# Kernel optimization log

Measured on AMD Instinct MI355X. Metric: run time of the kernel, lower is better.

Reference implementation:

```python
import jax, jax.numpy as jnp
import numpy as np

B, NPQ, NPV, NSL, K, ED, H = 64, 1024, 256, 1, 128, 16, 8
DK = K // H  # per-head dim (k_dim = v_dim = emb_dim // num_heads)
ETYPES = [("PQ","PQ"),("PQ","PV"),("PQ","Slack"),("PV","PQ"),("PV","PV"),("PV","Slack"),("Slack","PQ"),("Slack","PV")]
ECOUNTS = [262144, 131072, 4096, 131072, 65536, 2048, 4096, 2048]
NN = {"PQ": B*NPQ, "PV": B*NPV, "Slack": B*NSL}
LN_EPS = 1e-5


def setup_inputs() -> dict:
    ks = iter(jax.random.split(jax.random.key(0), 64))
    inp = {}
    for name, n in [("x_PQ", NN["PQ"]), ("x_PV", NN["PV"]), ("x_Slack", NN["Slack"])]:
        inp[name] = jax.random.normal(next(ks), (n, K), jnp.float32)
    for t, ((s, d), E) in enumerate(zip(ETYPES, ECOUNTS)):
        src = jax.random.randint(next(ks), (E,), 0, NN[s])
        dst = jax.random.randint(next(ks), (E,), 0, NN[d])
        inp[f"ei_{t}"] = jnp.stack([src, dst]).astype(jnp.int32)
        inp[f"ea_{t}"] = jax.random.normal(next(ks), (E, ED), jnp.float32)
    sc = 1.0 / np.sqrt(K)
    shapes = {"Wk": (2,8,K,K), "bk": (2,8,K), "Wq": (2,8,K,K), "bq": (2,8,K),
              "Wv": (2,8,K,K), "bv": (2,8,K), "Ws": (2,8,K,K), "bconv": (2,8,K),
              "We": (2,8,ED,K), "be": (2,8,K), "Wgt": (K,K), "bgt": (K,),
              "Wq1": (K,K), "Wk2": (K,K), "Wv2": (K,K), "Wo": (K,K), "bo": (K,)}
    for name, sh in shapes.items():
        inp[name] = jax.random.normal(next(ks), sh, jnp.float32) * sc
    inp["ln_g"] = jnp.ones((K,), jnp.float32)
    inp["ln_b"] = jnp.zeros((K,), jnp.float32)
    return inp


def _cross_attention(x1, x2, Wq1, Wk2, Wv2, Wo, bo):
    # x1: [B, N1, K] queries; x2: [B, N2, K] keys/values
    Bq, N1, _ = x1.shape
    N2 = x2.shape[1]
    q = (x1 @ Wq1).reshape(Bq, N1, H, DK)
    k = (x2 @ Wk2).reshape(Bq, N2, H, DK)
    v = (x2 @ Wv2).reshape(Bq, N2, H, DK)
    attn = jnp.einsum("bnhd,bmhd->bhnm", q, k) / np.sqrt(DK).astype(np.float32)
    attn = jax.nn.softmax(attn, axis=-1)
    out = jnp.einsum("bhnm,bmhd->bnhd", attn, v).reshape(Bq, N1, H * DK)
    return out @ Wo + bo


def _forward(x_PQ, x_PV, x_Slack, ei, ea,
             Wk, bk, Wq, bq, Wv, bv, Ws, bconv, We, be,
             Wgt, bgt, Wq1, Wk2, Wv2, Wo, bo, ln_g, ln_b):
    x = {"PQ": x_PQ, "PV": x_PV, "Slack": x_Slack}
    # global feature from input node features
    gf = jnp.concatenate([x_PQ.reshape(B, NPQ, K),
                          x_PV.reshape(B, NPV, K),
                          x_Slack.reshape(B, NSL, K)], axis=1)
    gf = gf @ Wgt + bgt
    gnode = jnp.concatenate([gf.mean(axis=1, keepdims=True),
                             gf.max(axis=1, keepdims=True)], axis=1)  # [B, 2, K]
    # 2 HeteroConv layers of ResGatedGraphConv, aggr='sum' over edge types
    for l in range(2):
        new = {t: jnp.zeros((NN[t], K), x_PQ.dtype) for t in ("PQ", "PV", "Slack")}
        for t, (s, d) in enumerate(ETYPES):
            xs, xd = x[s], x[d]
            k_ = xd @ Wk[l, t] + bk[l, t]   # lin_key on dst
            q_ = xs @ Wq[l, t] + bq[l, t]   # lin_query on src
            v_ = xs @ Wv[l, t] + bv[l, t]   # lin_value on src
            e_ = ea[t] @ We[l, t] + be[l, t]  # lin_edge
            si, di = ei[t][0], ei[t][1]
            gate = jax.nn.sigmoid(k_[di] + q_[si] + e_)  # [E, K]
            agg = jax.ops.segment_sum(gate * v_[si], di, num_segments=NN[d])
            new[d] = new[d] + agg + xd @ Ws[l, t] + bconv[l, t]
        x = {t: jax.nn.relu(v) for t, v in new.items()}
    # cross-attention vs. global mean/max nodes, residual, layernorm (PQ, PV only)
    res = {}
    for key2, N1 in (("PQ", NPQ), ("PV", NPV)):
        x1 = x[key2].reshape(B, N1, K)
        ca = _cross_attention(x1, gnode, Wq1, Wk2, Wv2, Wo, bo).reshape(B * N1, K)
        h = x[key2] + ca
        mu = h.mean(axis=-1, keepdims=True)
        var = ((h - mu) ** 2).mean(axis=-1, keepdims=True)
        res[key2] = (h - mu) * jax.lax.rsqrt(var + LN_EPS) * ln_g + ln_b
    return res["PQ"], res["PV"], x["Slack"]


def reference(x_PQ, x_PV, x_Slack,
              ei_0, ei_1, ei_2, ei_3, ei_4, ei_5, ei_6, ei_7,
              ea_0, ea_1, ea_2, ea_3, ea_4, ea_5, ea_6, ea_7,
              Wk, bk, Wq, bq, Wv, bv, Ws, bconv, We, be,
              Wgt, bgt, Wq1, Wk2, Wv2, Wo, bo, ln_g, ln_b):
    ei = [ei_0, ei_1, ei_2, ei_3, ei_4, ei_5, ei_6, ei_7]
    ea = [ea_0, ea_1, ea_2, ea_3, ea_4, ea_5, ea_6, ea_7]
    return _forward(x_PQ, x_PV, x_Slack, ei, ea,
                    Wk, bk, Wq, bq, Wv, bv, Ws, bconv, We, be,
                    Wgt, bgt, Wq1, Wk2, Wv2, Wo, bo, ln_g, ln_b)
```

## Files before the change

kernel.cpp:

```cpp
#include <hip/hip_runtime.h>
#include <hip/hip_bf16.h>
#include <math.h>

#define N_PQ 65536
#define N_PV 16384
#define N_SL 64

typedef __attribute__((ext_vector_type(8))) short s16x8;
typedef __attribute__((ext_vector_type(4))) float f32x4;

__device__ __forceinline__ ushort f2bf(float f) {
    union { float f; unsigned u; } x; x.f = f;
    unsigned r = x.u + 0x7fff + ((x.u >> 16) & 1);
    return (ushort)(r >> 16);
}
__device__ __forceinline__ float bf2f(ushort u) {
    union { unsigned u; float f; } x; x.u = ((unsigned)u) << 16;
    return x.f;
}

template<int OUT_BF16>
__global__ __launch_bounds__(256) void gemm_mfma(
    const ushort* __restrict__ A, const ushort* __restrict__ Bt,
    const float* __restrict__ bias, void* __restrict__ Cv, int M, int N)
{
    __shared__ ushort As[128 * 128];
    const int tid = threadIdx.x;
    const int m0 = blockIdx.x * 128;
    const int n0 = blockIdx.y * 128;

    #pragma unroll
    for (int p = 0; p < 8; ++p) {
        int c = p * 256 + tid;
        int row = c >> 4, c16 = c & 15;
        int gr = m0 + row;
        int4 v = make_int4(0, 0, 0, 0);
        if (gr < M) v = *(const int4*)(A + (size_t)gr * 128 + c16 * 8);
        *(int4*)(As + row * 128 + (c16 ^ (row & 7)) * 8) = v;
    }
    __syncthreads();

    const int lane = tid & 63, wave = tid >> 6;
    const int wr = wave >> 1, wc = wave & 1;
    const int lrow = lane & 15, lk = lane >> 4;

    f32x4 acc[4][4];
    #pragma unroll
    for (int mi = 0; mi < 4; ++mi)
        #pragma unroll
        for (int ni = 0; ni < 4; ++ni) acc[mi][ni] = (f32x4){0.f, 0.f, 0.f, 0.f};

    #pragma unroll
    for (int kk = 0; kk < 4; ++kk) {
        s16x8 a[4], b[4];
        #pragma unroll
        for (int mi = 0; mi < 4; ++mi) {
            int row = wr * 64 + mi * 16 + lrow;
            int c16 = (lk + kk * 4) ^ (row & 7);
            a[mi] = *(const s16x8*)(As + row * 128 + c16 * 8);
        }
        #pragma unroll
        for (int ni = 0; ni < 4; ++ni) {
            int n = n0 + wc * 64 + ni * 16 + lrow;
            b[ni] = *(const s16x8*)(Bt + (size_t)n * 128 + kk * 32 + lk * 8);
        }
        #pragma unroll
        for (int mi = 0; mi < 4; ++mi)
            #pragma unroll
            for (int ni = 0; ni < 4; ++ni)
                acc[mi][ni] = __builtin_amdgcn_mfma_f32_16x16x32_bf16(
                    a[mi], b[ni], acc[mi][ni], 0, 0, 0);
    }

    if (OUT_BF16) {
        __syncthreads();
        ushort* Cl = As;
        #pragma unroll
        for (int mi = 0; mi < 4; ++mi)
            #pragma unroll
            for (int ni = 0; ni < 4; ++ni)
                #pragma unroll
                for (int r = 0; r < 4; ++r) {
                    int row = wr * 64 + mi * 16 + (lane >> 4) * 4 + r;
                    int col = wc * 64 + ni * 16 + (lane & 15);
                    float v = acc[mi][ni][r] + (bias ? bias[n0 + col] : 0.f);
                    Cl[row * 128 + (((col >> 3) ^ (row & 7)) << 3) + (col & 7)] = f2bf(v);
                }
        __syncthreads();
        ushort* C = (ushort*)Cv;
        #pragma unroll
        for (int p = 0; p < 8; ++p) {
            int c = p * 256 + tid;
            int row = c >> 4, c16 = c & 15;
            int gr = m0 + row;
            if (gr < M)
                *(int4*)(C + (size_t)gr * N + n0 + c16 * 8) =
                    *(const int4*)(As + row * 128 + (c16 ^ (row & 7)) * 8);
        }
    } else {
        float* C = (float*)Cv;
        #pragma unroll
        for (int mi = 0; mi < 4; ++mi)
            #pragma unroll
            for (int ni = 0; ni < 4; ++ni)
                #pragma unroll
                for (int r = 0; r < 4; ++r) {
                    int row = m0 + wr * 64 + mi * 16 + (lane >> 4) * 4 + r;
                    int col = n0 + wc * 64 + ni * 16 + (lane & 15);
                    if (row < M)
                        C[(size_t)row * N + col] =
                            acc[mi][ni][r] + (bias ? bias[col] : 0.f);
                }
    }
}

__global__ void prep_mats(
    const float* __restrict__ Wk, const float* __restrict__ Wq,
    const float* __restrict__ Wv, const float* __restrict__ Ws,
    const float* __restrict__ Wgt, const float* __restrict__ Wq1,
    const float* __restrict__ Wk2, const float* __restrict__ Wv2,
    const float* __restrict__ Wo,
    ushort* __restrict__ panels, ushort* __restrict__ wssum,
    ushort* __restrict__ finalw)
{
    const int m = blockIdx.x >> 6;
    const int e = (blockIdx.x & 63) * 256 + threadIdx.x;
    const int nl = e >> 7, k = e & 127;
    const int dstlist[3][3] = {{0,3,6},{1,4,7},{2,5,-1}};
    const int srclist[3][3] = {{0,1,2},{3,4,5},{6,7,-1}};
    const int nkg[3] = {3,3,2};
    const int gofs[3] = {0,1280,2560};

    if (m < 52) {
        int l = m / 26, r = m % 26;
        int g, slot;
        if (r < 10)      { g = 0; slot = r; }
        else if (r < 20) { g = 1; slot = r - 10; }
        else             { g = 2; slot = r - 20; }
        int nk = nkg[g];
        float val; int col;
        if (slot < nk) {
            int t = dstlist[g][slot];
            val = Wk[(size_t)(l * 8 + t) * 16384 + k * 128 + nl];
            col = slot * 128 + nl;
        } else if (slot < 2 * nk) {
            int s = slot - nk; int t = srclist[g][s];
            val = Wq[(size_t)(l * 8 + t) * 16384 + k * 128 + nl];
            col = nk * 128 + s * 256 + ((nl >> 1) << 2) + (nl & 1);
        } else if (slot < 3 * nk) {
            int s = slot - 2 * nk; int t = srclist[g][s];
            val = Wv[(size_t)(l * 8 + t) * 16384 + k * 128 + nl];
            col = nk * 128 + s * 256 + ((nl >> 1) << 2) + 2 + (nl & 1);
        } else {
            float s = 0.f;
            #pragma unroll
            for (int i = 0; i < 3; ++i) {
                int t = dstlist[g][i];
                if (t >= 0) s += Ws[(size_t)(l * 8 + t) * 16384 + k * 128 + nl];
            }
            val = s; col = 1152 + nl;
        }
        panels[((size_t)l * 3328 + gofs[g] + col) * 128 + k] = f2bf(val);
    } else if (m < 54) {
        int l = m - 52;
        float s = Ws[(size_t)(l * 8 + 2) * 16384 + k * 128 + nl]
                + Ws[(size_t)(l * 8 + 5) * 16384 + k * 128 + nl];
        wssum[(size_t)l * 16384 + nl * 128 + k] = f2bf(s);
    } else {
        const float* fsrc[5] = {Wgt, Wq1, Wk2, Wv2, Wo};
        int idx = m - 54;
        finalw[(size_t)idx * 16384 + nl * 128 + k] = f2bf(fsrc[idx][k * 128 + nl]);
    }
}

__global__ void prep_bias(
    const float* __restrict__ bk, const float* __restrict__ bq,
    const float* __restrict__ bv, const float* __restrict__ bconv,
    float* __restrict__ bias_cat, float* __restrict__ bcsum)
{
    const int l = blockIdx.x / 3, g = blockIdx.x % 3;
    const int dstlist[3][3] = {{0,3,6},{1,4,7},{2,5,-1}};
    const int srclist[3][3] = {{0,1,2},{3,4,5},{6,7,-1}};
    const int nkg[3] = {3,3,2};
    const int gofs[3] = {0,1280,2560};
    const int nslots = (g < 2) ? 10 : 6;
    int nk = nkg[g];
    for (int idx = threadIdx.x; idx < nslots * 128; idx += 256) {
        int slot = idx >> 7, nl = idx & 127;
        float val; int col;
        if (slot < nk) {
            int t = dstlist[g][slot];
            val = bk[(l * 8 + t) * 128 + nl];
            col = slot * 128 + nl;
        } else if (slot < 2 * nk) {
            int s = slot - nk; int t = srclist[g][s];
            val = bq[(l * 8 + t) * 128 + nl];
            col = nk * 128 + s * 256 + ((nl >> 1) << 2) + (nl & 1);
        } else if (slot < 3 * nk) {
            int s = slot - 2 * nk; int t = srclist[g][s];
            val = bv[(l * 8 + t) * 128 + nl];
            col = nk * 128 + s * 256 + ((nl >> 1) << 2) + 2 + (nl & 1);
        } else {
            float s = 0.f;
            #pragma unroll
            for (int i = 0; i < 3; ++i) {
                int t = dstlist[g][i];
                if (t >= 0) s += bconv[(l * 8 + t) * 128 + nl];
            }
            val = s; col = 1152 + nl;
        }
        bias_cat[l * 3328 + gofs[g] + col] = val;
    }
    if (g == 2 && threadIdx.x < 128) {
        bcsum[l * 128 + threadIdx.x] =
            bconv[(l * 8 + 2) * 128 + threadIdx.x] + bconv[(l * 8 + 5) * 128 + threadIdx.x];
    }
}

struct HArgs {
    const int* ei[6];
    int E[6];
    int base[6];
    int cum[7];
};

__global__ void hist_kernel(HArgs A, int* __restrict__ bins)
{
    int g = blockIdx.x * 256 + threadIdx.x;
    if (g >= A.cum[6]) return;
    int t = 0;
    #pragma unroll
    for (int i = 0; i < 5; ++i) t += (g >= A.cum[i + 1]);
    int e = g - A.cum[t];
    int dst = A.ei[t][A.E[t] + e];
    atomicAdd(&bins[A.base[t] + dst], 1);
}

__global__ __launch_bounds__(256) void scan_a(
    const int* __restrict__ bins, int* __restrict__ offs, int* __restrict__ bsum)
{
    __shared__ int s[256];
    const int b = blockIdx.x, t = threadIdx.x;
    int v = bins[b * 256 + t];
    s[t] = v; __syncthreads();
    #pragma unroll
    for (int off = 1; off < 256; off <<= 1) {
        int x = (t >= off) ? s[t - off] : 0;
        __syncthreads();
        s[t] += x;
        __syncthreads();
    }
    offs[b * 256 + t] = s[t] - v;
    if (t == 255) bsum[b] = s[255];
}

__global__ __launch_bounds__(1024) void scan_b(
    const int* __restrict__ bsum, int* __restrict__ carry)
{
    __shared__ int s[1024];
    const int t = threadIdx.x;
    int v = bsum[t];
    s[t] = v; __syncthreads();
    for (int off = 1; off < 1024; off <<= 1) {
        int x = (t >= off) ? s[t - off] : 0;
        __syncthreads();
        s[t] += x;
        __syncthreads();
    }
    carry[t] = s[t] - v;
}

__global__ void scan_c(int* __restrict__ offs, const int* __restrict__ carry,
                       int* __restrict__ cursor)
{
    const int b = blockIdx.x, t = threadIdx.x;
    int v = offs[b * 256 + t] + carry[b];
    offs[b * 256 + t] = v;
    cursor[b * 256 + t] = v;
}

__global__ void scatter_kernel(HArgs A, int* __restrict__ cursor,
                               int* __restrict__ lsrc, int* __restrict__ leid)
{
    int g = blockIdx.x * 256 + threadIdx.x;
    if (g >= A.cum[6]) return;
    int t = 0;
    #pragma unroll
    for (int i = 0; i < 5; ++i) t += (g >= A.cum[i + 1]);
    int e = g - A.cum[t];
    int src = A.ei[t][e];
    int dst = A.ei[t][A.E[t] + e];
    int pos = atomicAdd(&cursor[A.base[t] + dst], 1);
    lsrc[pos] = src;
    leid[pos] = e;
}

struct GTA {
    int base, kcol, qvcol, lds;
    const ushort* Ys;
    const float* ea;
    const float* We;
    const float* be;
};
struct GArgs {
    GTA t[3];
    const int* offs;
    const int* lsrc;
    const int* leid;
    ushort* xbg;
    const ushort* Yg;
    int ldg, wscol;
};

__global__ __launch_bounds__(256) void gather_kernel(GArgs A)
{
    const int wave = threadIdx.x >> 6, lane = threadIdx.x & 63;
    const int d = blockIdx.x * 4 + wave;
    const int j0 = lane * 2;

    ushort2 w2 = *(const ushort2*)(A.Yg + (size_t)d * A.ldg + A.wscol + j0);
    float a0 = bf2f(w2.x), a1 = bf2f(w2.y);

    #pragma unroll
    for (int i = 0; i < 3; ++i) {
        const GTA T = A.t[i];
        int start = __builtin_amdgcn_readfirstlane(A.offs[T.base + d]);
        int end   = __builtin_amdgcn_readfirstlane(A.offs[T.base + d + 1]);
        if (start == end) continue;

        ushort2 kk = *(const ushort2*)(A.Yg + (size_t)d * A.ldg + T.kcol + j0);
        float k0 = bf2f(kk.x), k1 = bf2f(kk.y);
        float we0[16], we1[16];
        #pragma unroll
        for (int r = 0; r < 16; ++r) {
            float2 wv = *(const float2*)(T.We + r * 128 + j0);
            we0[r] = wv.x; we1[r] = wv.y;
        }
        float2 be2 = *(const float2*)(T.be + j0);

        int si  = __builtin_amdgcn_readfirstlane(A.lsrc[start]);
        int eid = __builtin_amdgcn_readfirstlane(A.leid[start]);
        uint2 qv = *(const uint2*)(T.Ys + (size_t)si * T.lds + T.qvcol + lane * 4);
        float4 eA = *(const float4*)(T.ea + (size_t)eid * 16);
        float4 eB = *(const float4*)(T.ea + (size_t)eid * 16 + 4);
        float4 eC = *(const float4*)(T.ea + (size_t)eid * 16 + 8);
        float4 eD = *(const float4*)(T.ea + (size_t)eid * 16 + 12);

        for (int e = start; e < end; ++e) {
            int nx = (e + 1 < end) ? (e + 1) : e;
            int si_n  = __builtin_amdgcn_readfirstlane(A.lsrc[nx]);
            int eid_n = __builtin_amdgcn_readfirstlane(A.leid[nx]);
            uint2 qv_n = *(const uint2*)(T.Ys + (size_t)si_n * T.lds + T.qvcol + lane * 4);
            float4 nA = *(const float4*)(T.ea + (size_t)eid_n * 16);
            float4 nB = *(const float4*)(T.ea + (size_t)eid_n * 16 + 4);
            float4 nC = *(const float4*)(T.ea + (size_t)eid_n * 16 + 8);
            float4 nD = *(const float4*)(T.ea + (size_t)eid_n * 16 + 12);

            float e0 = be2.x, e1 = be2.y;
            e0 += eA.x*we0[0] + eA.y*we0[1] + eA.z*we0[2] + eA.w*we0[3]
                + eB.x*we0[4] + eB.y*we0[5] + eB.z*we0[6] + eB.w*we0[7]
                + eC.x*we0[8] + eC.y*we0[9] + eC.z*we0[10] + eC.w*we0[11]
                + eD.x*we0[12] + eD.y*we0[13] + eD.z*we0[14] + eD.w*we0[15];
            e1 += eA.x*we1[0] + eA.y*we1[1] + eA.z*we1[2] + eA.w*we1[3]
                + eB.x*we1[4] + eB.y*we1[5] + eB.z*we1[6] + eB.w*we1[7]
                + eC.x*we1[8] + eC.y*we1[9] + eC.z*we1[10] + eC.w*we1[11]
                + eD.x*we1[12] + eD.y*we1[13] + eD.z*we1[14] + eD.w*we1[15];
            float q0 = bf2f((ushort)(qv.x & 0xffff)), q1 = bf2f((ushort)(qv.x >> 16));
            float v0 = bf2f((ushort)(qv.y & 0xffff)), v1 = bf2f((ushort)(qv.y >> 16));
            float g0 = 1.f / (1.f + __expf(-(k0 + q0 + e0)));
            float g1 = 1.f / (1.f + __expf(-(k1 + q1 + e1)));
            a0 += g0 * v0;
            a1 += g1 * v1;
            qv = qv_n; eA = nA; eB = nB; eC = nC; eD = nD;
        }
    }
    ushort2 o; o.x = f2bf(fmaxf(a0, 0.f)); o.y = f2bf(fmaxf(a1, 0.f));
    *(ushort2*)(A.xbg + (size_t)d * 128 + j0) = o;
}

__global__ __launch_bounds__(256) void edge_slack(
    const int* __restrict__ ei, const float* __restrict__ ea,
    const float* __restrict__ We, const float* __restrict__ be,
    const ushort* __restrict__ Yk, int ldk,
    const ushort* __restrict__ Yqv, int ldq,
    float* __restrict__ nd, int E)
{
    const int e = blockIdx.x * 2 + (threadIdx.x >> 7);
    if (e >= E) return;
    const int j = threadIdx.x & 127;
    const int si = ei[e];
    const int di = ei[E + e];

    float ej = be[j];
    #pragma unroll
    for (int r = 0; r < 16; ++r)
        ej += ea[(size_t)e * 16 + r] * We[r * 128 + j];

    float kv = bf2f(Yk[(size_t)di * ldk + j]);
    float qv = bf2f(Yqv[(size_t)si * ldq + ((j >> 1) << 2) + (j & 1)]);
    float vv = bf2f(Yqv[(size_t)si * ldq + ((j >> 1) << 2) + 2 + (j & 1)]);
    float g  = 1.f / (1.f + __expf(-(kv + qv + ej)));
    atomicAdd(&nd[(size_t)di * 128 + j], g * vv);
}

__global__ void f2b_kernel(const float* __restrict__ a, ushort* __restrict__ o, int n)
{
    int i = (blockIdx.x * 256 + threadIdx.x) * 4;
    if (i < n) {
        float4 v = *(const float4*)(a + i);
        ushort4 u; u.x = f2bf(v.x); u.y = f2bf(v.y); u.z = f2bf(v.z); u.w = f2bf(v.w);
        *(ushort4*)(o + i) = u;
    }
}
__global__ void relu_b_kernel(const float* __restrict__ a, ushort* __restrict__ o, int n)
{
    int i = (blockIdx.x * 256 + threadIdx.x) * 4;
    if (i < n) {
        float4 v = *(const float4*)(a + i);
        ushort4 u;
        u.x = f2bf(fmaxf(v.x, 0.f)); u.y = f2bf(fmaxf(v.y, 0.f));
        u.z = f2bf(fmaxf(v.z, 0.f)); u.w = f2bf(fmaxf(v.w, 0.f));
        *(ushort4*)(o + i) = u;
    }
}
__global__ void b2f_kernel(const ushort* __restrict__ a, float* __restrict__ o, int n)
{
    int i = blockIdx.x * 256 + threadIdx.x;
    if (i < n) o[i] = bf2f(a[i]);
}

__global__ void pool1(const ushort* __restrict__ gf, float* __restrict__ pbuf)
{
    const int b = blockIdx.x >> 4, c = blockIdx.x & 15;
    const int j = threadIdx.x;
    float s = 0.f, m = -INFINITY;
    const ushort* pq = gf + (size_t)(b * 1024 + c * 64) * 128;
    for (int i = 0; i < 64; ++i) { float v = bf2f(pq[i * 128 + j]); s += v; m = fmaxf(m, v); }
    const ushort* pv = gf + (size_t)(N_PQ + b * 256 + c * 16) * 128;
    for (int i = 0; i < 16; ++i) { float v = bf2f(pv[i * 128 + j]); s += v; m = fmaxf(m, v); }
    if (c == 0) { float v = bf2f(gf[(size_t)(N_PQ + N_PV + b) * 128 + j]); s += v; m = fmaxf(m, v); }
    pbuf[(size_t)blockIdx.x * 256 + j] = s;
    pbuf[(size_t)blockIdx.x * 256 + 128 + j] = m;
}
__global__ void pool2(const float* __restrict__ pbuf, float* __restrict__ gnode)
{
    const int b = blockIdx.x, j = threadIdx.x;
    float s = 0.f, m = -INFINITY;
    for (int c = 0; c < 16; ++c) {
        s += pbuf[(size_t)(b * 16 + c) * 256 + j];
        m = fmaxf(m, pbuf[(size_t)(b * 16 + c) * 256 + 128 + j]);
    }
    gnode[(size_t)(b * 2) * 128 + j]     = s * (1.f / 1281.f);
    gnode[(size_t)(b * 2 + 1) * 128 + j] = m;
}

__global__ __launch_bounds__(256) void attn_kernel(
    const ushort* __restrict__ q, const float* __restrict__ k2,
    const float* __restrict__ v2, ushort* __restrict__ ao, int shift, int Ntot)
{
    const int n = blockIdx.x * 2 + (threadIdx.x >> 7);
    if (n >= Ntot) return;
    const int j = threadIdx.x & 127;
    const int b = n >> shift;
    const int h16 = j & ~15;

    const ushort* qn = q + (size_t)n * 128 + h16;
    const float* k0 = k2 + (size_t)(b * 2) * 128 + h16;
    const float* k1 = k2 + (size_t)(b * 2 + 1) * 128 + h16;
    float s0 = 0.f, s1 = 0.f;
    #pragma unroll
    for (int d = 0; d < 16; ++d) {
        float qq = bf2f(qn[d]); s0 += qq * k0[d]; s1 += qq * k1[d];
    }
    s0 *= 0.25f; s1 *= 0.25f;
    float m  = fmaxf(s0, s1);
    float a0 = __expf(s0 - m), a1 = __expf(s1 - m);
    float inv = 1.f / (a0 + a1);
    ao[(size_t)n * 128 + j] = f2bf(
        (a0 * v2[(size_t)(b * 2) * 128 + j] + a1 * v2[(size_t)(b * 2 + 1) * 128 + j]) * inv);
}

__global__ __launch_bounds__(256) void ln_kernel(
    const ushort* __restrict__ x, const float* __restrict__ ca,
    const float* __restrict__ g, const float* __restrict__ bb,
    float* __restrict__ out, int N)
{
    const int n = blockIdx.x * 4 + (threadIdx.x >> 6);
    if (n >= N) return;
    const int l = threadIdx.x & 63;
    const size_t base = (size_t)n * 128;
    float h0 = bf2f(x[base + l * 2])     + ca[base + l * 2];
    float h1 = bf2f(x[base + l * 2 + 1]) + ca[base + l * 2 + 1];
    float s  = h0 + h1;
    float ss = h0 * h0 + h1 * h1;
    #pragma unroll
    for (int o = 32; o; o >>= 1) { s += __shfl_xor(s, o); ss += __shfl_xor(ss, o); }
    float mu  = s * (1.f / 128.f);
    float var = ss * (1.f / 128.f) - mu * mu;
    float rs  = rsqrtf(var + 1e-5f);
    out[base + l * 2]     = (h0 - mu) * rs * g[l * 2]     + bb[l * 2];
    out[base + l * 2 + 1] = (h1 - mu) * rs * g[l * 2 + 1] + bb[l * 2 + 1];
}

extern "C" void kernel_launch(void* const* d_in, const int* in_sizes, int n_in,
                              void* d_out, int out_size, void* d_ws, size_t ws_size,
                              hipStream_t stream)
{
    const float* xin[3] = {(const float*)d_in[0], (const float*)d_in[1], (const float*)d_in[2]};
    const int NNs[3] = {N_PQ, N_PV, N_SL};
    const int ncol[3] = {1280, 1280, 768};
    const int gofs[3] = {0, 1280, 2560};

    const int*   ei[8];
    const float* ea[8];
    int          Ecnt[8];
    for (int t = 0; t < 8; ++t) {
        ei[t]   = (const int*)d_in[3 + 2 * t];
        ea[t]   = (const float*)d_in[4 + 2 * t];
        Ecnt[t] = in_sizes[3 + 2 * t] / 2;
    }
    const float* Wk    = (const float*)d_in[19];
    const float* bk    = (const float*)d_in[20];
    const float* Wq    = (const float*)d_in[21];
    const float* bq    = (const float*)d_in[22];
    const float* Wv    = (const float*)d_in[23];
    const float* bv    = (const float*)d_in[24];
    const float* Ws    = (const float*)d_in[25];
    const float* bconv = (const float*)d_in[26];
    const float* We    = (const float*)d_in[27];
    const float* be    = (const float*)d_in[28];
    const float* Wgt   = (const float*)d_in[29];
    const float* bgt   = (const float*)d_in[30];
    const float* Wq1   = (const float*)d_in[31];
    const float* Wk2   = (const float*)d_in[32];
    const float* Wv2   = (const float*)d_in[33];
    const float* Wo    = (const float*)d_in[34];
    const float* bo    = (const float*)d_in[35];
    const float* ln_g  = (const float*)d_in[36];
    const float* ln_b  = (const float*)d_in[37];

    char* w = (char*)d_ws;
    ushort* Y[3];
    Y[0] = (ushort*)w; w += (size_t)N_PQ * 1280 * 2;
    Y[1] = (ushort*)w; w += (size_t)N_PV * 1280 * 2;
    Y[2] = (ushort*)w; w += (size_t)N_SL * 768 * 2;
    ushort* xb[3];
    xb[0] = (ushort*)w; w += (size_t)N_PQ * 128 * 2;
    xb[1] = (ushort*)w; w += (size_t)N_PV * 128 * 2;
    xb[2] = (ushort*)w; w += (size_t)N_SL * 128 * 2;
    ushort* panels = (ushort*)w; w += (size_t)2 * 3328 * 128 * 2;
    ushort* wssum  = (ushort*)w; w += (size_t)2 * 16384 * 2;
    ushort* finalw = (ushort*)w; w += (size_t)5 * 16384 * 2;
    float* bias_cat = (float*)w; w += 6656 * 4;
    float* bcsum    = (float*)w; w += 256 * 4;
    float* gnode    = (float*)w; w += 16384 * 4;
    ushort* gnodeb  = (ushort*)w; w += 16384 * 2;
    float* k2       = (float*)w; w += 16384 * 4;
    float* v2       = (float*)w; w += 16384 * 4;
    float* pbuf     = (float*)w; w += 1024 * 256 * 4;
    const int NBINS = 262144;
    int* bins   = (int*)w; w += (size_t)NBINS * 4;
    int* offs   = (int*)w; w += (size_t)NBINS * 4;
    int* cursor = (int*)w; w += (size_t)NBINS * 4;
    int* bsum   = (int*)w; w += 1024 * 4;
    int* carry  = (int*)w; w += 1024 * 4;
    int* lsrc   = (int*)w; w += (size_t)600064 * 4;
    int* leid   = (int*)w; w += (size_t)600064 * 4;
    ushort* gf   = Y[0];
    ushort* qb   = Y[0];
    ushort* ao   = (ushort*)((char*)Y[0] + (size_t)N_PQ * 128 * 2);
    float*  cbuf = (float*)((char*)Y[0] + (size_t)N_PQ * 128 * 4);
    float* outp = (float*)d_out;
    float* nw2 = outp + (size_t)(N_PQ + N_PV) * 128;

    const ushort* Wgt_t = finalw;
    const ushort* Wq1_t = finalw + 16384;
    const ushort* Wk2_t = finalw + 32768;
    const ushort* Wv2_t = finalw + 49152;
    const ushort* Wo_t  = finalw + 65536;

    auto gemm_b = [&](const ushort* A, const ushort* Bt, const float* bias,
                      ushort* C, int M, int N) {
        gemm_mfma<1><<<dim3((M + 127) / 128, N / 128), 256, 0, stream>>>(A, Bt, bias, C, M, N);
    };
    auto gemm_f = [&](const ushort* A, const ushort* Bt, const float* bias,
                      float* C, int M, int N) {
        gemm_mfma<0><<<dim3((M + 127) / 128, N / 128), 256, 0, stream>>>(A, Bt, bias, C, M, N);
    };

    prep_mats<<<59 * 64, 256, 0, stream>>>(Wk, Wq, Wv, Ws, Wgt, Wq1, Wk2, Wv2, Wo,
                                           panels, wssum, finalw);
    prep_bias<<<6, 256, 0, stream>>>(bk, bq, bv, bconv, bias_cat, bcsum);
    for (int g = 0; g < 3; ++g) {
        int n = NNs[g] * 128;
        f2b_kernel<<<dim3((n / 4 + 255) / 256), 256, 0, stream>>>(xin[g], xb[g], n);
    }

    const int csr_t[6]    = {0, 3, 6, 1, 4, 7};
    const int csr_base[6] = {0, 65536, 131072, 196608, 212992, 229376};
    HArgs ha;
    {
        int c = 0;
        for (int i = 0; i < 6; ++i) {
            int t = csr_t[i];
            ha.ei[i] = ei[t]; ha.E[i] = Ecnt[t]; ha.base[i] = csr_base[i];
            ha.cum[i] = c; c += Ecnt[t];
        }
        ha.cum[6] = c;
    }
    hipMemsetAsync(bins, 0, (size_t)NBINS * 4, stream);
    hist_kernel<<<dim3((ha.cum[6] + 255) / 256), 256, 0, stream>>>(ha, bins);
    scan_a<<<1024, 256, 0, stream>>>(bins, offs, bsum);
    scan_b<<<1, 1024, 0, stream>>>(bsum, carry);
    scan_c<<<1024, 256, 0, stream>>>(offs, carry, cursor);
    scatter_kernel<<<dim3((ha.cum[6] + 255) / 256), 256, 0, stream>>>(ha, cursor, lsrc, leid);

    gemm_b(xb[0], Wgt_t, bgt, gf, N_PQ, 128);
    gemm_b(xb[1], Wgt_t, bgt, gf + (size_t)N_PQ * 128, N_PV, 128);
    gemm_b(xb[2], Wgt_t, bgt, gf + (size_t)(N_PQ + N_PV) * 128, N_SL, 128);
    pool1<<<1024, 128, 0, stream>>>(gf, pbuf);
    pool2<<<64, 128, 0, stream>>>(pbuf, gnode);
    f2b_kernel<<<dim3(16384 / 4 / 256), 256, 0, stream>>>(gnode, gnodeb, 16384);
    gemm_f(gnodeb, Wk2_t, nullptr, k2, 128, 128);
    gemm_f(gnodeb, Wv2_t, nullptr, v2, 128, 128);

    for (int l = 0; l < 2; ++l) {
        for (int g = 0; g < 3; ++g)
            gemm_b(xb[g], panels + ((size_t)l * 3328 + gofs[g]) * 128,
                   bias_cat + l * 3328 + gofs[g], Y[g], NNs[g], ncol[g]);
        gemm_f(xb[2], wssum + (size_t)l * 16384, bcsum + l * 128, nw2, N_SL, 128);

        for (int g = 0; g < 2; ++g) {
            GArgs ga;
            for (int i = 0; i < 3; ++i) {
                int t = csr_t[g * 3 + i], off = l * 8 + t;
                int sgrp = (i == 2) ? 2 : i;
                ga.t[i].base  = csr_base[g * 3 + i];
                ga.t[i].kcol  = i * 128;
                ga.t[i].lds   = ncol[sgrp];
                ga.t[i].qvcol = ((sgrp == 2) ? 256 : 384) + g * 256;
                ga.t[i].Ys    = Y[sgrp];
                ga.t[i].ea    = ea[t];
                ga.t[i].We    = We + (size_t)off * 2048;
                ga.t[i].be    = be + (size_t)off * 128;
            }
            ga.offs = offs; ga.lsrc = lsrc; ga.leid = leid;
            ga.xbg = xb[g]; ga.Yg = Y[g]; ga.ldg = ncol[g]; ga.wscol = 1152;
            gather_kernel<<<dim3(NNs[g] / 4), 256, 0, stream>>>(ga);
        }

        {
            int off2 = l * 8 + 2;
            edge_slack<<<dim3((Ecnt[2] + 1) / 2), 256, 0, stream>>>(
                ei[2], ea[2], We + (size_t)off2 * 2048, be + (size_t)off2 * 128,
                Y[2] + 0, 768, Y[0] + 896, 1280, nw2, Ecnt[2]);
            int off5 = l * 8 + 5;
            edge_slack<<<dim3((Ecnt[5] + 1) / 2), 256, 0, stream>>>(
                ei[5], ea[5], We + (size_t)off5 * 2048, be + (size_t)off5 * 128,
                Y[2] + 128, 768, Y[1] + 896, 1280, nw2, Ecnt[5]);
        }
        relu_b_kernel<<<dim3(8), 256, 0, stream>>>(nw2, xb[2], N_SL * 128);
    }

    gemm_b(xb[0], Wq1_t, nullptr, qb, N_PQ, 128);
    attn_kernel<<<dim3(N_PQ / 2), 256, 0, stream>>>(qb, k2, v2, ao, 10, N_PQ);
    gemm_f(ao, Wo_t, bo, cbuf, N_PQ, 128);
    ln_kernel<<<dim3(N_PQ / 4), 256, 0, stream>>>(xb[0], cbuf, ln_g, ln_b, outp, N_PQ);
    gemm_b(xb[1], Wq1_t, nullptr, qb, N_PV, 128);
    attn_kernel<<<dim3(N_PV / 2), 256, 0, stream>>>(qb, k2, v2, ao, 8, N_PV);
    gemm_f(ao, Wo_t, bo, cbuf, N_PV, 128);
    ln_kernel<<<dim3(N_PV / 4), 256, 0, stream>>>(xb[1], cbuf, ln_g, ln_b,
                                                  outp + (size_t)N_PQ * 128, N_PV);
    b2f_kernel<<<dim3((N_SL * 128 + 255) / 256), 256, 0, stream>>>(
        xb[2], outp + (size_t)(N_PQ + N_PV) * 128, N_SL * 128);
}
```

Measured before the change: 985.1 us.

## Widen GEMM N-tile, pack CSR src/eid pairs, stage edge weights in LDS

When N is a multiple of 256, the bf16-output GEMM now computes two 128-column tiles per block, so the A tile loaded into LDS is reused across more output columns. The CSR source and edge-id arrays are merged into one int2 array, so each edge needs a single index load. The gather kernel now stages all three edge-type We matrices in LDS instead of holding them in registers, and reads edge attributes per iteration rather than prefetching them. The trade-offs are doubled accumulator register pressure in the GEMM, 24 KB of LDS per gather block, and ea loads that are no longer prefetched one edge ahead.

```diff
diff --git a/kernel.cpp b/kernel.cpp
--- a/kernel.cpp
+++ b/kernel.cpp
@@ -19,7 +19,7 @@
     return x.f;
 }
 
-template<int OUT_BF16>
+template<int OUT_BF16, int NT>
 __global__ __launch_bounds__(256) void gemm_mfma(
     const ushort* __restrict__ A, const ushort* __restrict__ Bt,
     const float* __restrict__ bias, void* __restrict__ Cv, int M, int N)
@@ -27,7 +27,7 @@
     __shared__ ushort As[128 * 128];
     const int tid = threadIdx.x;
     const int m0 = blockIdx.x * 128;
-    const int n0 = blockIdx.y * 128;
+    const int n0 = blockIdx.y * (128 * NT);
 
     #pragma unroll
     for (int p = 0; p < 8; ++p) {
@@ -44,15 +44,15 @@
     const int wr = wave >> 1, wc = wave & 1;
     const int lrow = lane & 15, lk = lane >> 4;
 
-    f32x4 acc[4][4];
+    f32x4 acc[4][4 * NT];
     #pragma unroll
     for (int mi = 0; mi < 4; ++mi)
         #pragma unroll
-        for (int ni = 0; ni < 4; ++ni) acc[mi][ni] = (f32x4){0.f, 0.f, 0.f, 0.f};
+        for (int ni = 0; ni < 4 * NT; ++ni) acc[mi][ni] = (f32x4){0.f, 0.f, 0.f, 0.f};
 
     #pragma unroll
     for (int kk = 0; kk < 4; ++kk) {
-        s16x8 a[4], b[4];
+        s16x8 a[4], b[4 * NT];
         #pragma unroll
         for (int mi = 0; mi < 4; ++mi) {
             int row = wr * 64 + mi * 16 + lrow;
@@ -60,53 +60,57 @@
             a[mi] = *(const s16x8*)(As + row * 128 + c16 * 8);
         }
         #pragma unroll
-        for (int ni = 0; ni < 4; ++ni) {
-            int n = n0 + wc * 64 + ni * 16 + lrow;
+        for (int ni = 0; ni < 4 * NT; ++ni) {
+            int n = n0 + (ni >> 2) * 128 + wc * 64 + (ni & 3) * 16 + lrow;
             b[ni] = *(const s16x8*)(Bt + (size_t)n * 128 + kk * 32 + lk * 8);
         }
         #pragma unroll
         for (int mi = 0; mi < 4; ++mi)
             #pragma unroll
-            for (int ni = 0; ni < 4; ++ni)
+            for (int ni = 0; ni < 4 * NT; ++ni)
                 acc[mi][ni] = __builtin_amdgcn_mfma_f32_16x16x32_bf16(
                     a[mi], b[ni], acc[mi][ni], 0, 0, 0);
     }
 
     if (OUT_BF16) {
-        __syncthreads();
-        ushort* Cl = As;
         #pragma unroll
-        for (int mi = 0; mi < 4; ++mi)
+        for (int s = 0; s < NT; ++s) {
+            __syncthreads();
+            ushort* Cl = As;
             #pragma unroll
-            for (int ni = 0; ni < 4; ++ni)
+            for (int mi = 0; mi < 4; ++mi)
                 #pragma unroll
-                for (int r = 0; r < 4; ++r) {
-                    int row = wr * 64 + mi * 16 + (lane >> 4) * 4 + r;
-                    int col = wc * 64 + ni * 16 + (lane & 15);
-                    float v = acc[mi][ni][r] + (bias ? bias[n0 + col] : 0.f);
-                    Cl[row * 128 + (((col >> 3) ^ (row & 7)) << 3) + (col & 7)] = f2bf(v);
-                }
-        __syncthreads();
-        ushort* C = (ushort*)Cv;
-        #pragma unroll
-        for (int p = 0; p < 8; ++p) {
-            int c = p * 256 + tid;
-            int row = c >> 4, c16 = c & 15;
-            int gr = m0 + row;
-            if (gr < M)
-                *(int4*)(C + (size_t)gr * N + n0 + c16 * 8) =
-                    *(const int4*)(As + row * 128 + (c16 ^ (row & 7)) * 8);
+                for (int q = 0; q < 4; ++q)
+                    #pragma unroll
+                    for (int r = 0; r < 4; ++r) {
+                        int row = wr * 64 + mi * 16 + (lane >> 4) * 4 + r;
+                        int col = wc * 64 + q * 16 + (lane & 15);
+                        float v = acc[mi][s * 4 + q][r]
+                                + (bias ? bias[n0 + s * 128 + col] : 0.f);
+                        Cl[row * 128 + (((col >> 3) ^ (row & 7)) << 3) + (col & 7)] = f2bf(v);
+                    }
+            __syncthreads();
+            ushort* C = (ushort*)Cv;
+            #pragma unroll
+            for (int p = 0; p < 8; ++p) {
+                int c = p * 256 + tid;
+                int row = c >> 4, c16 = c & 15;
+                int gr = m0 + row;
+                if (gr < M)
+                    *(int4*)(C + (size_t)gr * N + n0 + s * 128 + c16 * 8) =
+                        *(const int4*)(As + row * 128 + (c16 ^ (row & 7)) * 8);
+            }
         }
     } else {
         float* C = (float*)Cv;
         #pragma unroll
         for (int mi = 0; mi < 4; ++mi)
             #pragma unroll
-            for (int ni = 0; ni < 4; ++ni)
+            for (int ni = 0; ni < 4 * NT; ++ni)
                 #pragma unroll
                 for (int r = 0; r < 4; ++r) {
                     int row = m0 + wr * 64 + mi * 16 + (lane >> 4) * 4 + r;
-                    int col = n0 + wc * 64 + ni * 16 + (lane & 15);
+                    int col = n0 + (ni >> 2) * 128 + wc * 64 + (ni & 3) * 16 + (lane & 15);
                     if (row < M)
                         C[(size_t)row * N + col] =
                             acc[mi][ni][r] + (bias ? bias[col] : 0.f);
@@ -280,7 +284,7 @@
 }
 
 __global__ void scatter_kernel(HArgs A, int* __restrict__ cursor,
-                               int* __restrict__ lsrc, int* __restrict__ leid)
+                               int2* __restrict__ lpair)
 {
     int g = blockIdx.x * 256 + threadIdx.x;
     if (g >= A.cum[6]) return;
@@ -291,8 +295,7 @@
     int src = A.ei[t][e];
     int dst = A.ei[t][A.E[t] + e];
     int pos = atomicAdd(&cursor[A.base[t] + dst], 1);
-    lsrc[pos] = src;
-    leid[pos] = e;
+    lpair[pos] = make_int2(src, e);
 }
 
 struct GTA {
@@ -305,8 +308,7 @@
 struct GArgs {
     GTA t[3];
     const int* offs;
-    const int* lsrc;
-    const int* leid;
+    const int2* lpair;
     ushort* xbg;
     const ushort* Yg;
     int ldg, wscol;
@@ -314,7 +316,13 @@
 
 __global__ __launch_bounds__(256) void gather_kernel(GArgs A)
 {
-    const int wave = threadIdx.x >> 6, lane = threadIdx.x & 63;
+    __shared__ float ldsWe[3 * 16 * 128];
+    const int tid = threadIdx.x;
+    for (int idx = tid; idx < 3 * 2048; idx += 256)
+        ldsWe[idx] = A.t[idx >> 11].We[idx & 2047];
+    __syncthreads();
+
+    const int wave = tid >> 6, lane = tid & 63;
     const int d = blockIdx.x * 4 + wave;
     const int j0 = lane * 2;
 
@@ -330,48 +338,37 @@
 
         ushort2 kk = *(const ushort2*)(A.Yg + (size_t)d * A.ldg + T.kcol + j0);
         float k0 = bf2f(kk.x), k1 = bf2f(kk.y);
-        float we0[16], we1[16];
-        #pragma unroll
-        for (int r = 0; r < 16; ++r) {
-            float2 wv = *(const float2*)(T.We + r * 128 + j0);
-            we0[r] = wv.x; we1[r] = wv.y;
-        }
         float2 be2 = *(const float2*)(T.be + j0);
-
-        int si  = __builtin_amdgcn_readfirstlane(A.lsrc[start]);
-        int eid = __builtin_amdgcn_readfirstlane(A.leid[start]);
+        const float* Wl = ldsWe + i * 2048;
+
+        int2 pr = A.lpair[start];
+        int si  = __builtin_amdgcn_readfirstlane(pr.x);
+        int eid = __builtin_amdgcn_readfirstlane(pr.y);
         uint2 qv = *(const uint2*)(T.Ys + (size_t)si * T.lds + T.qvcol + lane * 4);
-        float4 eA = *(const float4*)(T.ea + (size_t)eid * 16);
-        float4 eB = *(const float4*)(T.ea + (size_t)eid * 16 + 4);
-        float4 eC = *(const float4*)(T.ea + (size_t)eid * 16 + 8);
-        float4 eD = *(const float4*)(T.ea + (size_t)eid * 16 + 12);
 
         for (int e = start; e < end; ++e) {
+            const float* eap = T.ea + (size_t)eid * 16;
+            uint2 qv_c = qv;
             int nx = (e + 1 < end) ? (e + 1) : e;
-            int si_n  = __builtin_amdgcn_readfirstlane(A.lsrc[nx]);
-            int eid_n = __builtin_amdgcn_readfirstlane(A.leid[nx]);
-            uint2 qv_n = *(const uint2*)(T.Ys + (size_t)si_n * T.lds + T.qvcol + lane * 4);
-            float4 nA = *(const float4*)(T.ea + (size_t)eid_n * 16);
-            float4 nB = *(const float4*)(T.ea + (size_t)eid_n * 16 + 4);
-            float4 nC = *(const float4*)(T.ea + (size_t)eid_n * 16 + 8);
-            float4 nD = *(const float4*)(T.ea + (size_t)eid_n * 16 + 12);
+            int2 prn = A.lpair[nx];
+            int si_n = __builtin_amdgcn_readfirstlane(prn.x);
+            eid = __builtin_amdgcn_readfirstlane(prn.y);
+            qv = *(const uint2*)(T.Ys + (size_t)si_n * T.lds + T.qvcol + lane * 4);
 
             float e0 = be2.x, e1 = be2.y;
-            e0 += eA.x*we0[0] + eA.y*we0[1] + eA.z*we0[2] + eA.w*we0[3]
-                + eB.x*we0[4] + eB.y*we0[5] + eB.z*we0[6] + eB.w*we0[7]
-                + eC.x*we0[8] + eC.y*we0[9] + eC.z*we0[10] + eC.w*we0[11]
-                + eD.x*we0[12] + eD.y*we0[13] + eD.z*we0[14] + eD.w*we0[15];
-            e1 += eA.x*we1[0] + eA.y*we1[1] + eA.z*we1[2] + eA.w*we1[3]
-                + eB.x*we1[4] + eB.y*we1[5] + eB.z*we1[6] + eB.w*we1[7]
-                + eC.x*we1[8] + eC.y*we1[9] + eC.z*we1[10] + eC.w*we1[11]
-                + eD.x*we1[12] + eD.y*we1[13] + eD.z*we1[14] + eD.w*we1[15];
-            float q0 = bf2f((ushort)(qv.x & 0xffff)), q1 = bf2f((ushort)(qv.x >> 16));
-            float v0 = bf2f((ushort)(qv.y & 0xffff)), v1 = bf2f((ushort)(qv.y >> 16));
+            #pragma unroll
+            for (int r = 0; r < 16; ++r) {
+                float er = eap[r];
+                float2 wv = *(const float2*)(Wl + r * 128 + j0);
+                e0 = fmaf(er, wv.x, e0);
+                e1 = fmaf(er, wv.y, e1);
+            }
+            float q0 = bf2f((ushort)(qv_c.x & 0xffff)), q1 = bf2f((ushort)(qv_c.x >> 16));
+            float v0 = bf2f((ushort)(qv_c.y & 0xffff)), v1 = bf2f((ushort)(qv_c.y >> 16));
             float g0 = 1.f / (1.f + __expf(-(k0 + q0 + e0)));
             float g1 = 1.f / (1.f + __expf(-(k1 + q1 + e1)));
-            a0 += g0 * v0;
-            a1 += g1 * v1;
-            qv = qv_n; eA = nA; eB = nB; eC = nC; eD = nD;
+            a0 = fmaf(g0, v0, a0);
+            a1 = fmaf(g1, v1, a1);
         }
     }
     ushort2 o; o.x = f2bf(fmaxf(a0, 0.f)); o.y = f2bf(fmaxf(a1, 0.f));
@@ -564,8 +561,7 @@
     int* cursor = (int*)w; w += (size_t)NBINS * 4;
     int* bsum   = (int*)w; w += 1024 * 4;
     int* carry  = (int*)w; w += 1024 * 4;
-    int* lsrc   = (int*)w; w += (size_t)600064 * 4;
-    int* leid   = (int*)w; w += (size_t)600064 * 4;
+    int2* lpair = (int2*)w; w += (size_t)600064 * 8;
     ushort* gf   = Y[0];
     ushort* qb   = Y[0];
     ushort* ao   = (ushort*)((char*)Y[0] + (size_t)N_PQ * 128 * 2);
@@ -581,11 +577,17 @@
 
     auto gemm_b = [&](const ushort* A, const ushort* Bt, const float* bias,
                       ushort* C, int M, int N) {
-        gemm_mfma<1><<<dim3((M + 127) / 128, N / 128), 256, 0, stream>>>(A, Bt, bias, C, M, N);
+        if (N % 256 == 0)
+            gemm_mfma<1, 2><<<dim3((M + 127) / 128, N / 256), 256, 0, stream>>>(
+                A, Bt, bias, C, M, N);
+        else
+            gemm_mfma<1, 1><<<dim3((M + 127) / 128, N / 128), 256, 0, stream>>>(
+                A, Bt, bias, C, M, N);
     };
     auto gemm_f = [&](const ushort* A, const ushort* Bt, const float* bias,
                       float* C, int M, int N) {
-        gemm_mfma<0><<<dim3((M + 127) / 128, N / 128), 256, 0, stream>>>(A, Bt, bias, C, M, N);
+        gemm_mfma<0, 1><<<dim3((M + 127) / 128, N / 128), 256, 0, stream>>>(
+            A, Bt, bias, C, M, N);
     };
 
     prep_mats<<<59 * 64, 256, 0, stream>>>(Wk, Wq, Wv, Ws, Wgt, Wq1, Wk2, Wv2, Wo,
@@ -613,7 +615,7 @@
     scan_a<<<1024, 256, 0, stream>>>(bins, offs, bsum);
     scan_b<<<1, 1024, 0, stream>>>(bsum, carry);
     scan_c<<<1024, 256, 0, stream>>>(offs, carry, cursor);
-    scatter_kernel<<<dim3((ha.cum[6] + 255) / 256), 256, 0, stream>>>(ha, cursor, lsrc, leid);
+    scatter_kernel<<<dim3((ha.cum[6] + 255) / 256), 256, 0, stream>>>(ha, cursor, lpair);
 
     gemm_b(xb[0], Wgt_t, bgt, gf, N_PQ, 128);
     gemm_b(xb[1], Wgt_t, bgt, gf + (size_t)N_PQ * 128, N_PV, 128);
@@ -644,7 +646,7 @@
                 ga.t[i].We    = We + (size_t)off * 2048;
                 ga.t[i].be    = be + (size_t)off * 128;
             }
-            ga.offs = offs; ga.lsrc = lsrc; ga.leid = leid;
+            ga.offs = offs; ga.lpair = lpair;
             ga.xbg = xb[g]; ga.Yg = Y[g]; ga.ldg = ncol[g]; ga.wscol = 1152;
             gather_kernel<<<dim3(NNs[g] / 4), 256, 0, stream>>>(ga);
         }
```

After: 1.408 ms. 1.43x slower.

## Interleave q/v columns per channel, pack CSR src/eid pairs, one channel per thread in gather

Applied to the files above, without the earlier changes.

Changes the weight-panel layout so each output channel's q and v values sit next to each other, letting the gather and slack-edge kernels read them with a single ushort2 load. Merges the separate lsrc/leid CSR arrays into one int2 array, so each edge needs one load instead of two. Restructures the gather kernel so each thread handles one channel, with two destination nodes per block instead of four, and sets a launch bound of 4 blocks per CU. The goal is better occupancy and fewer index loads, at the cost of more threads and more redundant per-edge loads of the edge attributes.

```diff
diff --git a/kernel.cpp b/kernel.cpp
--- a/kernel.cpp
+++ b/kernel.cpp
@@ -146,11 +146,11 @@
         } else if (slot < 2 * nk) {
             int s = slot - nk; int t = srclist[g][s];
             val = Wq[(size_t)(l * 8 + t) * 16384 + k * 128 + nl];
-            col = nk * 128 + s * 256 + ((nl >> 1) << 2) + (nl & 1);
+            col = nk * 128 + s * 256 + nl * 2;
         } else if (slot < 3 * nk) {
             int s = slot - 2 * nk; int t = srclist[g][s];
             val = Wv[(size_t)(l * 8 + t) * 16384 + k * 128 + nl];
-            col = nk * 128 + s * 256 + ((nl >> 1) << 2) + 2 + (nl & 1);
+            col = nk * 128 + s * 256 + nl * 2 + 1;
         } else {
             float s = 0.f;
             #pragma unroll
@@ -195,11 +195,11 @@
         } else if (slot < 2 * nk) {
             int s = slot - nk; int t = srclist[g][s];
             val = bq[(l * 8 + t) * 128 + nl];
-            col = nk * 128 + s * 256 + ((nl >> 1) << 2) + (nl & 1);
+            col = nk * 128 + s * 256 + nl * 2;
         } else if (slot < 3 * nk) {
             int s = slot - 2 * nk; int t = srclist[g][s];
             val = bv[(l * 8 + t) * 128 + nl];
-            col = nk * 128 + s * 256 + ((nl >> 1) << 2) + 2 + (nl & 1);
+            col = nk * 128 + s * 256 + nl * 2 + 1;
         } else {
             float s = 0.f;
             #pragma unroll
@@ -280,7 +280,7 @@
 }
 
 __global__ void scatter_kernel(HArgs A, int* __restrict__ cursor,
-                               int* __restrict__ lsrc, int* __restrict__ leid)
+                               int2* __restrict__ lpair)
 {
     int g = blockIdx.x * 256 + threadIdx.x;
     if (g >= A.cum[6]) return;
@@ -291,8 +291,7 @@
     int src = A.ei[t][e];
     int dst = A.ei[t][A.E[t] + e];
     int pos = atomicAdd(&cursor[A.base[t] + dst], 1);
-    lsrc[pos] = src;
-    leid[pos] = e;
+    lpair[pos] = make_int2(src, e);
 }
 
 struct GTA {
@@ -305,21 +304,19 @@
 struct GArgs {
     GTA t[3];
     const int* offs;
-    const int* lsrc;
-    const int* leid;
+    const int2* lpair;
     ushort* xbg;
     const ushort* Yg;
     int ldg, wscol;
 };
 
-__global__ __launch_bounds__(256) void gather_kernel(GArgs A)
-{
-    const int wave = threadIdx.x >> 6, lane = threadIdx.x & 63;
-    const int d = blockIdx.x * 4 + wave;
-    const int j0 = lane * 2;
-
-    ushort2 w2 = *(const ushort2*)(A.Yg + (size_t)d * A.ldg + A.wscol + j0);
-    float a0 = bf2f(w2.x), a1 = bf2f(w2.y);
+__global__ __launch_bounds__(256, 4) void gather_kernel(GArgs A)
+{
+    const int half = threadIdx.x >> 7;
+    const int j    = threadIdx.x & 127;
+    const int d = blockIdx.x * 2 + half;
+
+    float acc = bf2f(A.Yg[(size_t)d * A.ldg + A.wscol + j]);
 
     #pragma unroll
     for (int i = 0; i < 3; ++i) {
@@ -328,54 +325,50 @@
         int end   = __builtin_amdgcn_readfirstlane(A.offs[T.base + d + 1]);
         if (start == end) continue;
 
-        ushort2 kk = *(const ushort2*)(A.Yg + (size_t)d * A.ldg + T.kcol + j0);
-        float k0 = bf2f(kk.x), k1 = bf2f(kk.y);
-        float we0[16], we1[16];
-        #pragma unroll
-        for (int r = 0; r < 16; ++r) {
-            float2 wv = *(const float2*)(T.We + r * 128 + j0);
-            we0[r] = wv.x; we1[r] = wv.y;
-        }
-        float2 be2 = *(const float2*)(T.be + j0);
-
-        int si  = __builtin_amdgcn_readfirstlane(A.lsrc[start]);
-        int eid = __builtin_amdgcn_readfirstlane(A.leid[start]);
-        uint2 qv = *(const uint2*)(T.Ys + (size_t)si * T.lds + T.qvcol + lane * 4);
+        float kj  = bf2f(A.Yg[(size_t)d * A.ldg + T.kcol + j]);
+        float bej = T.be[j];
+        float wec[16];
+        #pragma unroll
+        for (int r = 0; r < 16; ++r) wec[r] = T.We[r * 128 + j];
+
+        int2 pr = A.lpair[start];
+        int si  = __builtin_amdgcn_readfirstlane(pr.x);
+        int eid = __builtin_amdgcn_readfirstlane(pr.y);
+        ushort2 qv = *(const ushort2*)(T.Ys + (size_t)si * T.lds + T.qvcol + j * 2);
         float4 eA = *(const float4*)(T.ea + (size_t)eid * 16);
         float4 eB = *(const float4*)(T.ea + (size_t)eid * 16 + 4);
         float4 eC = *(const float4*)(T.ea + (size_t)eid * 16 + 8);
         float4 eD = *(const float4*)(T.ea + (size_t)eid * 16 + 12);
 
         for (int e = start; e < end; ++e) {
+            ushort2 qv_c = qv;
+            float4 cA = eA, cB = eB, cC = eC, cD = eD;
             int nx = (e + 1 < end) ? (e + 1) : e;
-            int si_n  = __builtin_amdgcn_readfirstlane(A.lsrc[nx]);
-            int eid_n = __builtin_amdgcn_readfirstlane(A.leid[nx]);
-            uint2 qv_n = *(const uint2*)(T.Ys + (size_t)si_n * T.lds + T.qvcol + lane * 4);
-            float4 nA = *(const float4*)(T.ea + (size_t)eid_n * 16);
-            float4 nB = *(const float4*)(T.ea + (size_t)eid_n * 16 + 4);
-            float4 nC = *(const float4*)(T.ea + (size_t)eid_n * 16 + 8);
-            float4 nD = *(const float4*)(T.ea + (size_t)eid_n * 16 + 12);
-
-            float e0 = be2.x, e1 = be2.y;
-            e0 += eA.x*we0[0] + eA.y*we0[1] + eA.z*we0[2] + eA.w*we0[3]
-                + eB.x*we0[4] + eB.y*we0[5] + eB.z*we0[6] + eB.w*we0[7]
-                + eC.x*we0[8] + eC.y*we0[9] + eC.z*we0[10] + eC.w*we0[11]
-                + eD.x*we0[12] + eD.y*we0[13] + eD.z*we0[14] + eD.w*we0[15];
-            e1 += eA.x*we1[0] + eA.y*we1[1] + eA.z*we1[2] + eA.w*we1[3]
-                + eB.x*we1[4] + eB.y*we1[5] + eB.z*we1[6] + eB.w*we1[7]
-                + eC.x*we1[8] + eC.y*we1[9] + eC.z*we1[10] + eC.w*we1[11]
-                + eD.x*we1[12] + eD.y*we1[13] + eD.z*we1[14] + eD.w*we1[15];
-            float q0 = bf2f((ushort)(qv.x & 0xffff)), q1 = bf2f((ushort)(qv.x >> 16));
-            float v0 = bf2f((ushort)(qv.y & 0xffff)), v1 = bf2f((ushort)(qv.y >> 16));
-            float g0 = 1.f / (1.f + __expf(-(k0 + q0 + e0)));
-            float g1 = 1.f / (1.f + __expf(-(k1 + q1 + e1)));
-            a0 += g0 * v0;
-            a1 += g1 * v1;
-            qv = qv_n; eA = nA; eB = nB; eC = nC; eD = nD;
-        }
-    }
-    ushort2 o; o.x = f2bf(fmaxf(a0, 0.f)); o.y = f2bf(fmaxf(a1, 0.f));
-    *(ushort2*)(A.xbg + (size_t)d * 128 + j0) = o;
+            int2 prn = A.lpair[nx];
+            int si_n = __builtin_amdgcn_readfirstlane(prn.x);
+            eid = __builtin_amdgcn_readfirstlane(prn.y);
+            qv = *(const ushort2*)(T.Ys + (size_t)si_n * T.lds + T.qvcol + j * 2);
+            eA = *(const float4*)(T.ea + (size_t)eid * 16);
+            eB = *(const float4*)(T.ea + (size_t)eid * 16 + 4);
+            eC = *(const float4*)(T.ea + (size_t)eid * 16 + 8);
+            eD = *(const float4*)(T.ea + (size_t)eid * 16 + 12);
+
+            float ej = bej;
+            ej = fmaf(cA.x, wec[0],  ej); ej = fmaf(cA.y, wec[1],  ej);
+            ej = fmaf(cA.z, wec[2],  ej); ej = fmaf(cA.w, wec[3],  ej);
+            ej = fmaf(cB.x, wec[4],  ej); ej = fmaf(cB.y, wec[5],  ej);
+            ej = fmaf(cB.z, wec[6],  ej); ej = fmaf(cB.w, wec[7],  ej);
+            ej = fmaf(cC.x, wec[8],  ej); ej = fmaf(cC.y, wec[9],  ej);
+            ej = fmaf(cC.z, wec[10], ej); ej = fmaf(cC.w, wec[11], ej);
+            ej = fmaf(cD.x, wec[12], ej); ej = fmaf(cD.y, wec[13], ej);
+            ej = fmaf(cD.z, wec[14], ej); ej = fmaf(cD.w, wec[15], ej);
+
+            float q = bf2f(qv_c.x), v = bf2f(qv_c.y);
+            float g = 1.f / (1.f + __expf(-(kj + q + ej)));
+            acc = fmaf(g, v, acc);
+        }
+    }
+    A.xbg[(size_t)d * 128 + j] = f2bf(fmaxf(acc, 0.f));
 }
 
 __global__ __launch_bounds__(256) void edge_slack(
@@ -397,10 +390,9 @@
         ej += ea[(size_t)e * 16 + r] * We[r * 128 + j];
 
     float kv = bf2f(Yk[(size_t)di * ldk + j]);
-    float qv = bf2f(Yqv[(size_t)si * ldq + ((j >> 1) << 2) + (j & 1)]);
-    float vv = bf2f(Yqv[(size_t)si * ldq + ((j >> 1) << 2) + 2 + (j & 1)]);
-    float g  = 1.f / (1.f + __expf(-(kv + qv + ej)));
-    atomicAdd(&nd[(size_t)di * 128 + j], g * vv);
+    ushort2 qv = *(const ushort2*)(Yqv + (size_t)si * ldq + j * 2);
+    float g  = 1.f / (1.f + __expf(-(kv + bf2f(qv.x) + ej)));
+    atomicAdd(&nd[(size_t)di * 128 + j], g * bf2f(qv.y));
 }
 
 __global__ void f2b_kernel(const float* __restrict__ a, ushort* __restrict__ o, int n)
@@ -564,8 +556,7 @@
     int* cursor = (int*)w; w += (size_t)NBINS * 4;
     int* bsum   = (int*)w; w += 1024 * 4;
     int* carry  = (int*)w; w += 1024 * 4;
-    int* lsrc   = (int*)w; w += (size_t)600064 * 4;
-    int* leid   = (int*)w; w += (size_t)600064 * 4;
+    int2* lpair = (int2*)w; w += (size_t)600064 * 8;
     ushort* gf   = Y[0];
     ushort* qb   = Y[0];
     ushort* ao   = (ushort*)((char*)Y[0] + (size_t)N_PQ * 128 * 2);
@@ -613,7 +604,7 @@
     scan_a<<<1024, 256, 0, stream>>>(bins, offs, bsum);
     scan_b<<<1, 1024, 0, stream>>>(bsum, carry);
     scan_c<<<1024, 256, 0, stream>>>(offs, carry, cursor);
-    scatter_kernel<<<dim3((ha.cum[6] + 255) / 256), 256, 0, stream>>>(ha, cursor, lsrc, leid);
+    scatter_kernel<<<dim3((ha.cum[6] + 255) / 256), 256, 0, stream>>>(ha, cursor, lpair);
 
     gemm_b(xb[0], Wgt_t, bgt, gf, N_PQ, 128);
     gemm_b(xb[1], Wgt_t, bgt, gf + (size_t)N_PQ * 128, N_PV, 128);
@@ -644,20 +635,20 @@
                 ga.t[i].We    = We + (size_t)off * 2048;
                 ga.t[i].be    = be + (size_t)off * 128;
             }
-            ga.offs = offs; ga.lsrc = lsrc; ga.leid = leid;
+            ga.offs = offs; ga.lpair = lpair;
             ga.xbg = xb[g]; ga.Yg = Y[g]; ga.ldg = ncol[g]; ga.wscol = 1152;
-            gather_kernel<<<dim3(NNs[g] / 4), 256, 0, stream>>>(ga);
+            gather_kernel<<<dim3(NNs[g] / 2), 256, 0, stream>>>(ga);
         }
 
         {
             int off2 = l * 8 + 2;
             edge_slack<<<dim3((Ecnt[2] + 1) / 2), 256, 0, stream>>>(
                 ei[2], ea[2], We + (size_t)off2 * 2048, be + (size_t)off2 * 128,
-                Y[2] + 0, 768, Y[0] + 896, 1280, nw2, Ecnt[2]);
+                Y[2] + 0, 768, Y[0] + 384 + 512, 1280, nw2, Ecnt[2]);
             int off5 = l * 8 + 5;
             edge_slack<<<dim3((Ecnt[5] + 1) / 2), 256, 0, stream>>>(
                 ei[5], ea[5], We + (size_t)off5 * 2048, be + (size_t)off5 * 128,
-                Y[2] + 128, 768, Y[1] + 896, 1280, nw2, Ecnt[5]);
+                Y[2] + 128, 768, Y[1] + 384 + 512, 1280, nw2, Ecnt[5]);
         }
         relu_b_kernel<<<dim3(8), 256, 0, stream>>>(nw2, xb[2], N_SL * 128);
     }
@@ -666,11 +657,13 @@
     attn_kernel<<<dim3(N_PQ / 2), 256, 0, stream>>>(qb, k2, v2, ao, 10, N_PQ);
     gemm_f(ao, Wo_t, bo, cbuf, N_PQ, 128);
     ln_kernel<<<dim3(N_PQ / 4), 256, 0, stream>>>(xb[0], cbuf, ln_g, ln_b, outp, N_PQ);
+
     gemm_b(xb[1], Wq1_t, nullptr, qb, N_PV, 128);
     attn_kernel<<<dim3(N_PV / 2), 256, 0, stream>>>(qb, k2, v2, ao, 8, N_PV);
     gemm_f(ao, Wo_t, bo, cbuf, N_PV, 128);
     ln_kernel<<<dim3(N_PV / 4), 256, 0, stream>>>(xb[1], cbuf, ln_g, ln_b,
                                                   outp + (size_t)N_PQ * 128, N_PV);
+
     b2f_kernel<<<dim3((N_SL * 128 + 255) / 256), 256, 0, stream>>>(
         xb[2], outp + (size_t)(N_PQ + N_PV) * 128, N_SL * 128);
 }
```

Result: no change. 1.004 ms (+2.0%).
